# Kernel optimization log

Hardware: AMD Instinct MI355X
Metric: run time of the kernel (lower is better)

## Reference

```python
import jax, jax.numpy as jnp
import numpy as np

B, S, H = 4, 2048, 2048


def _rotate_half(x):
    x1, x2 = jnp.split(x, 2, axis=-1)
    return jnp.concatenate((-x2, x1), axis=-1)


def _rope_tables(seq_len, dim, dtype):
    # standard RoPE over the full hidden dim (emb last dim == dim so it
    # broadcasts against [B,S,dim] activations)
    inv_freq = 1.0 / (10000.0 ** (jnp.arange(0, dim, 2, dtype=jnp.float32) / dim))
    t = jnp.arange(seq_len, dtype=jnp.float32)
    freqs = jnp.einsum('s,d->sd', t, inv_freq)          # [S, dim/2]
    emb = jnp.concatenate((freqs, freqs), axis=-1)      # [S, dim]
    return jnp.cos(emb).astype(dtype)[None], jnp.sin(emb).astype(dtype)[None]  # [1,S,dim]


def setup_inputs() -> dict:
    key = jax.random.key(0)
    ks = jax.random.split(key, 11)
    sc = 0.02
    return {
        'query': jax.random.normal(ks[0], (B, S, H), jnp.float32),
        'key':   jax.random.normal(ks[1], (B, S, H), jnp.float32),
        'value': jax.random.normal(ks[2], (B, S, H), jnp.float32),
        'Wq': jax.random.normal(ks[3], (H, H), jnp.float32) * sc,
        'bq': jax.random.normal(ks[4], (H,), jnp.float32) * sc,
        'Wk': jax.random.normal(ks[5], (H, H), jnp.float32) * sc,
        'bk': jax.random.normal(ks[6], (H,), jnp.float32) * sc,
        'Wv': jax.random.normal(ks[7], (H, H), jnp.float32) * sc,
        'bv': jax.random.normal(ks[8], (H,), jnp.float32) * sc,
        'Wo': jax.random.normal(ks[9], (H, H), jnp.float32) * sc,
        'bo': jax.random.normal(ks[10], (H,), jnp.float32) * sc,
    }


def reference(query, key, value, Wq, bq, Wk, bk, Wv, bv, Wo, bo):
    seq, dim = query.shape[1], query.shape[2]
    cos, sin = _rope_tables(seq, dim, query.dtype)      # [1,S,H]
    q_rot = query * cos + _rotate_half(query) * sin     # RoPE BEFORE projections
    k_rot = key * cos + _rotate_half(key) * sin
    q = jnp.einsum('bsh,oh->bso', q_rot, Wq) + bq       # torch Linear: x @ W.T + b
    k = jnp.einsum('bsh,oh->bso', k_rot, Wk) + bk
    v = jnp.einsum('bsh,oh->bso', value, Wv) + bv
    scale = 1.0 / jnp.sqrt(jnp.asarray(dim, q.dtype))
    scores = jnp.einsum('bqh,bkh->bqk', q, k) * scale   # [B,Sq,Sk]
    probs = jax.nn.softmax(scores, axis=-1)
    context = jnp.einsum('bqk,bkh->bqh', probs, v)
    return jnp.einsum('bsh,oh->bso', context, Wo) + bo
```

## Files before the change

### kernel.cpp

```cpp
#include <hip/hip_runtime.h>


typedef __bf16 bf16_t;
typedef bf16_t bf16x8 __attribute__((ext_vector_type(8)));
typedef bf16_t bf16x4 __attribute__((ext_vector_type(4)));
typedef float  f32x4  __attribute__((ext_vector_type(4)));

#define BDIM 4
#define SDIM 2048
#define HDIM 2048

__device__ __forceinline__ void async_copy16(const bf16_t* g, bf16_t* l) {
  __builtin_amdgcn_global_load_lds(
      (__attribute__((address_space(1))) const void*)g,
      (__attribute__((address_space(3))) void*)l,
      16, 0, 0);
}

__global__ __launch_bounds__(256) void prep_kernel(
    const float* __restrict__ q, const float* __restrict__ k,
    const float* __restrict__ v,
    bf16_t* __restrict__ qr, bf16_t* __restrict__ kr, bf16_t* __restrict__ vb) {
  const int i = blockIdx.x * 256 + threadIdx.x;
  const int j = i & 1023;
  const int row = i >> 10;
  const int s = row & (SDIM - 1);
  const float invf = exp2f(-(float)j * 0.012976281620653759f);
  const float f = (float)s * invf;
  float sn, cs;
  sincosf(f, &sn, &cs);
  const long base = (long)row * HDIM;
  const float q1 = q[base + j], q2 = q[base + j + 1024];
  const float k1 = k[base + j], k2 = k[base + j + 1024];
  qr[base + j]        = (bf16_t)(q1 * cs - q2 * sn);
  qr[base + j + 1024] = (bf16_t)(q2 * cs + q1 * sn);
  kr[base + j]        = (bf16_t)(k1 * cs - k2 * sn);
  kr[base + j + 1024] = (bf16_t)(k2 * cs + k1 * sn);
  vb[base + j]        = (bf16_t)v[base + j];
  vb[base + j + 1024] = (bf16_t)v[base + j + 1024];
}

__global__ __launch_bounds__(256) void wcast_kernel(
    const float* __restrict__ w0, const float* __restrict__ w1,
    const float* __restrict__ w2, const float* __restrict__ w3,
    bf16_t* __restrict__ dst) {
  const int wsel = blockIdx.y;
  const float* src = wsel == 0 ? w0 : wsel == 1 ? w1 : wsel == 2 ? w2 : w3;
  const long i = (long)(blockIdx.x * 256 + threadIdx.x) * 8;
  const float4 a = *(const float4*)&src[i];
  const float4 b = *(const float4*)&src[i + 4];
  bf16x8 o;
  o[0] = (bf16_t)a.x; o[1] = (bf16_t)a.y; o[2] = (bf16_t)a.z; o[3] = (bf16_t)a.w;
  o[4] = (bf16_t)b.x; o[5] = (bf16_t)b.y; o[6] = (bf16_t)b.z; o[7] = (bf16_t)b.w;
  *(bf16x8*)&dst[(long)wsel * HDIM * HDIM + i] = o;
}

__device__ __forceinline__ void stage_A_unit(const bf16_t* __restrict__ G, int K,
                                             int kq, bf16_t* L, int half,
                                             int wave, int rl, int ccs) {
#pragma unroll
  for (int c = 0; c < 2; ++c) {
    const int idx = c * 8 + wave;
    const int g = (idx >> 3) * 16 + (idx & 7) + half * 8;
    async_copy16(G + (long)(g * 8 + rl) * K + kq + ccs, L + g * 512);
  }
}
__device__ __forceinline__ void stage_B_unit(const bf16_t* __restrict__ G, int K,
                                             int kq, bf16_t* L, int half,
                                             int wave, int rl, int ccs) {
#pragma unroll
  for (int c = 0; c < 2; ++c) {
    const int idx = c * 8 + wave;
    const int g = (idx >> 2) * 8 + (idx & 3) + half * 4;
    async_copy16(G + (long)(g * 8 + rl) * K + kq + ccs, L + g * 512);
  }
}

template <int OMODE>
__global__ __launch_bounds__(512, 2) void gemm_bt(
    const bf16_t* __restrict__ A, const bf16_t* __restrict__ Bt,
    void* __restrict__ Cv, const float* __restrict__ bias,
    int M, int N, int K, float alpha,
    long sA, long sB, long sC) {
  __shared__ __align__(16) bf16_t lds[4 * 16384];
  bf16_t* As0 = lds;
  bf16_t* Bs0 = lds + 16384;
  bf16_t* As1 = lds + 32768;
  bf16_t* Bs1 = lds + 49152;
  const int z = blockIdx.z;
  A  += (long)z * sA;
  Bt += (long)z * sB;
  const int tid  = threadIdx.x;
  const int lane = tid & 63;
  const int wave = tid >> 6;
  const int wm = (wave >> 2) * 128;
  const int wn = (wave & 3) * 64;
  const int m0 = blockIdx.y * 256;
  const int n0 = blockIdx.x * 256;
  const int lrow = lane & 15;
  const int quad = lane >> 4;
  const int rl  = lane >> 3;
  const int ccs = ((lane & 7) ^ rl) * 8;

  const bf16_t* Ab = A  + (long)m0 * K;
  const bf16_t* Bb = Bt + (long)n0 * K;

  f32x4 acc[8][4] = {};

#define DS_A(AS, MH)                                                         \
  _Pragma("unroll") for (int ks = 0; ks < 2; ++ks) {                         \
    const int cg = ks * 4 + quad;                                            \
    _Pragma("unroll") for (int t = 0; t < 4; ++t) {                          \
      const int r = wm + ((MH) * 4 + t) * 16 + lrow;                         \
      af[t][ks] = *(const bf16x8*)&(AS)[r * 64 + ((cg ^ (r & 7)) * 8)];      \
    }                                                                        \
  }
#define DS_B(BS, NH)                                                         \
  _Pragma("unroll") for (int ks = 0; ks < 2; ++ks) {                         \
    const int cg = ks * 4 + quad;                                            \
    _Pragma("unroll") for (int u = 0; u < 2; ++u) {                          \
      const int r = wn + ((NH) * 2 + u) * 16 + lrow;                         \
      bfr[u][ks] = *(const bf16x8*)&(BS)[r * 64 + ((cg ^ (r & 7)) * 8)];     \
    }                                                                        \
  }
#define MFMA_Q(MH, NH)                                                       \
  __builtin_amdgcn_s_barrier();                                              \
  asm volatile("s_waitcnt lgkmcnt(0)" ::: "memory");                         \
  __builtin_amdgcn_s_setprio(1);                                             \
  _Pragma("unroll") for (int ks = 0; ks < 2; ++ks)                           \
    _Pragma("unroll") for (int t = 0; t < 4; ++t)                            \
      _Pragma("unroll") for (int u = 0; u < 2; ++u)                          \
        acc[(MH) * 4 + t][(NH) * 2 + u] =                                    \
            __builtin_amdgcn_mfma_f32_16x16x32_bf16(                         \
                af[t][ks], bfr[u][ks], acc[(MH) * 4 + t][(NH) * 2 + u],      \
                0, 0, 0);                                                    \
  __builtin_amdgcn_s_setprio(0);
#define VM_WAIT4 asm volatile("s_waitcnt vmcnt(4)" ::: "memory");
#define ENDBAR   __builtin_amdgcn_s_barrier();

  stage_A_unit(Ab, K, 0,  As0, 0, wave, rl, ccs);
  stage_A_unit(Ab, K, 0,  As0, 1, wave, rl, ccs);
  stage_B_unit(Bb, K, 0,  Bs0, 0, wave, rl, ccs);
  stage_B_unit(Bb, K, 0,  Bs0, 1, wave, rl, ccs);
  stage_A_unit(Ab, K, 64, As1, 0, wave, rl, ccs);
  stage_B_unit(Bb, K, 64, Bs1, 0, wave, rl, ccs);
  asm volatile("s_waitcnt vmcnt(4)" ::: "memory");
  __builtin_amdgcn_s_barrier();

  const int Km = K - 1;
  for (int k0 = 0; k0 < K; k0 += 128) {
    bf16x8 af[4][2], bfr[2][2];
    const int kA = k0 + 64;
    const int kB = (k0 + 128) & Km;
    const int kC = (k0 + 192) & Km;
    DS_A(As0, 0) DS_B(Bs0, 0)
    stage_A_unit(Ab, K, kA, As1, 1, wave, rl, ccs);
    MFMA_Q(0, 0) ENDBAR
    DS_B(Bs0, 1)
    stage_B_unit(Bb, K, kA, Bs1, 1, wave, rl, ccs);
    MFMA_Q(0, 1) ENDBAR
    DS_A(As0, 1) DS_B(Bs0, 0)
    stage_A_unit(Ab, K, kB, As0, 0, wave, rl, ccs);
    MFMA_Q(1, 0) ENDBAR
    DS_B(Bs0, 1)
    stage_B_unit(Bb, K, kB, Bs0, 0, wave, rl, ccs);
    MFMA_Q(1, 1) VM_WAIT4 ENDBAR
    DS_A(As1, 0) DS_B(Bs1, 0)
    stage_A_unit(Ab, K, kB, As0, 1, wave, rl, ccs);
    MFMA_Q(0, 0) ENDBAR
    DS_B(Bs1, 1)
    stage_B_unit(Bb, K, kB, Bs0, 1, wave, rl, ccs);
    MFMA_Q(0, 1) ENDBAR
    DS_A(As1, 1) DS_B(Bs1, 0)
    stage_A_unit(Ab, K, kC, As1, 0, wave, rl, ccs);
    MFMA_Q(1, 0) ENDBAR
    DS_B(Bs1, 1)
    stage_B_unit(Bb, K, kC, Bs1, 0, wave, rl, ccs);
    MFMA_Q(1, 1) VM_WAIT4 ENDBAR
  }
#undef DS_A
#undef DS_B
#undef MFMA_Q
#undef VM_WAIT4
#undef ENDBAR

#pragma unroll
  for (int mt = 0; mt < 8; ++mt) {
#pragma unroll
    for (int nt = 0; nt < 4; ++nt) {
      const int col = n0 + wn + nt * 16 + lrow;
      const float bv = bias ? bias[col] : 0.0f;
      if (OMODE == 2) {
        const int row0 = m0 + wm + mt * 16 + quad * 4;
        const int b = row0 >> 11;
        const int s = row0 & (SDIM - 1);
        bf16x4 o;
#pragma unroll
        for (int r = 0; r < 4; ++r) o[r] = (bf16_t)(acc[mt][nt][r] + bv);
        *(bf16x4*)&((bf16_t*)Cv)[(long)b * SDIM * HDIM + (long)col * SDIM + s] = o;
      } else {
#pragma unroll
        for (int r = 0; r < 4; ++r) {
          const int row = m0 + wm + mt * 16 + quad * 4 + r;
          const float v = acc[mt][nt][r] * alpha + bv;
          if (OMODE == 1)
            ((float*)Cv)[(long)z * sC + (long)row * N + col] = v;
          else
            ((bf16_t*)Cv)[(long)z * sC + (long)row * N + col] = (bf16_t)v;
        }
      }
    }
  }
}

__global__ __launch_bounds__(256) void softmax_kernel(
    const bf16_t* __restrict__ Sc, bf16_t* __restrict__ P) {
  const long row = blockIdx.x;
  const bf16_t* src = Sc + row * SDIM;
  bf16_t* dst = P + row * SDIM;
  const int tid = threadIdx.x;
  const bf16x8 in = *(const bf16x8*)&src[tid * 8];
  float x[8];
#pragma unroll
  for (int t = 0; t < 8; ++t) x[t] = (float)in[t];
  float m = x[0];
#pragma unroll
  for (int t = 1; t < 8; ++t) m = fmaxf(m, x[t]);
#pragma unroll
  for (int off = 32; off; off >>= 1) m = fmaxf(m, __shfl_xor(m, off));
  __shared__ float redm[4], reds[4];
  const int wave = tid >> 6, lane = tid & 63;
  if (lane == 0) redm[wave] = m;
  __syncthreads();
  m = fmaxf(fmaxf(redm[0], redm[1]), fmaxf(redm[2], redm[3]));
  float s = 0.0f;
#pragma unroll
  for (int t = 0; t < 8; ++t) { x[t] = __expf(x[t] - m); s += x[t]; }
#pragma unroll
  for (int off = 32; off; off >>= 1) s += __shfl_xor(s, off);
  if (lane == 0) reds[wave] = s;
  __syncthreads();
  s = reds[0] + reds[1] + reds[2] + reds[3];
  const float inv = 1.0f / s;
  bf16x8 o;
#pragma unroll
  for (int t = 0; t < 8; ++t) o[t] = (bf16_t)(x[t] * inv);
  *(bf16x8*)&dst[tid * 8] = o;
}

extern "C" void kernel_launch(void* const* d_in, const int* in_sizes, int n_in,
                              void* d_out, int out_size, void* d_ws, size_t ws_size,
                              hipStream_t stream) {
  const float* q_in = (const float*)d_in[0];
  const float* k_in = (const float*)d_in[1];
  const float* v_in = (const float*)d_in[2];
  const float* Wq = (const float*)d_in[3];
  const float* bq = (const float*)d_in[4];
  const float* Wk = (const float*)d_in[5];
  const float* bk = (const float*)d_in[6];
  const float* Wv = (const float*)d_in[7];
  const float* bv = (const float*)d_in[8];
  const float* Wo = (const float*)d_in[9];
  const float* bo = (const float*)d_in[10];
  float* out = (float*)d_out;

  const size_t ELE  = (size_t)BDIM * SDIM * HDIM;
  const size_t WELE = (size_t)HDIM * HDIM;
  const size_t SEG  = ELE * 2;

  uint8_t* w = (uint8_t*)d_ws;
  bf16_t* qr  = (bf16_t*)(w + 0 * SEG);
  bf16_t* kr  = (bf16_t*)(w + 1 * SEG);
  bf16_t* vb  = (bf16_t*)(w + 2 * SEG);
  bf16_t* Wb  = (bf16_t*)(w + 3 * SEG);
  bf16_t* qp  = (bf16_t*)(w + 4 * SEG);
  bf16_t* kp  = (bf16_t*)(w + 5 * SEG);
  bf16_t* vpT = (bf16_t*)(w + 6 * SEG);
  bf16_t* scores = (bf16_t*)(w + 0 * SEG);
  bf16_t* probs  = (bf16_t*)(w + 2 * SEG);
  bf16_t* ctx    = (bf16_t*)(w + 1 * SEG);

  bf16_t* Wqb = Wb + 0 * WELE;
  bf16_t* Wkb = Wb + 1 * WELE;
  bf16_t* Wvb = Wb + 2 * WELE;
  bf16_t* Wob = Wb + 3 * WELE;

  const dim3 blk(256);
  const dim3 gblk(512);
  const long SH = (long)SDIM * HDIM;
  const long SS = (long)SDIM * SDIM;

  prep_kernel<<<dim3(ELE / 2 / 256), blk, 0, stream>>>(q_in, k_in, v_in, qr, kr, vb);
  wcast_kernel<<<dim3(WELE / 8 / 256, 4), blk, 0, stream>>>(Wq, Wk, Wv, Wo, Wb);
  gemm_bt<0><<<dim3(8, 32, 1), gblk, 0, stream>>>(qr, Wqb, qp, bq,
      BDIM * SDIM, HDIM, HDIM, 1.0f, 0, 0, 0);
  gemm_bt<0><<<dim3(8, 32, 1), gblk, 0, stream>>>(kr, Wkb, kp, bk,
      BDIM * SDIM, HDIM, HDIM, 1.0f, 0, 0, 0);
  gemm_bt<2><<<dim3(8, 32, 1), gblk, 0, stream>>>(vb, Wvb, vpT, bv,
      BDIM * SDIM, HDIM, HDIM, 1.0f, 0, 0, 0);
  gemm_bt<0><<<dim3(8, 8, BDIM), gblk, 0, stream>>>(qp, kp, scores, nullptr,
      SDIM, SDIM, HDIM, 0.022097086912079612f, SH, SH, SS);
  softmax_kernel<<<dim3(BDIM * SDIM), blk, 0, stream>>>(scores, probs);
  gemm_bt<0><<<dim3(8, 8, BDIM), gblk, 0, stream>>>(probs, vpT, ctx, nullptr,
      SDIM, HDIM, SDIM, 1.0f, SS, SH, SH);
  gemm_bt<1><<<dim3(8, 32, 1), gblk, 0, stream>>>(ctx, Wob, out, bo,
      BDIM * SDIM, HDIM, HDIM, 1.0f, 0, 0, 0);
}
```

Baseline: 653.7 us.

## Stage GEMM epilogue through LDS for coalesced vector global stores

For non-transposed outputs the MFMA operands are swapped so each lane holds four consecutive columns, which enables vector bias loads. Every wave then writes its accumulator tile into a padded per-wave LDS scratch region. It reads the tile back as row-contiguous 16-byte chunks and issues coalesced global stores, replacing the scalar strided stores of the previous epilogue. The shared buffer grows to 144 KiB, so occupancy may drop from two blocks per CU.

```diff
diff --git a/kernel.cpp b/kernel.cpp
--- a/kernel.cpp
+++ b/kernel.cpp
@@ -82,11 +82,11 @@
     void* __restrict__ Cv, const float* __restrict__ bias,
     int M, int N, int K, float alpha,
     long sA, long sB, long sC) {
-  __shared__ __align__(16) bf16_t lds[4 * 16384];
-  bf16_t* As0 = lds;
-  bf16_t* Bs0 = lds + 16384;
-  bf16_t* As1 = lds + 32768;
-  bf16_t* Bs1 = lds + 49152;
+  __shared__ __align__(16) uint8_t smem[147456];
+  bf16_t* As0 = (bf16_t*)smem;
+  bf16_t* Bs0 = (bf16_t*)(smem + 32768);
+  bf16_t* As1 = (bf16_t*)(smem + 65536);
+  bf16_t* Bs1 = (bf16_t*)(smem + 98304);
   const int z = blockIdx.z;
   A  += (long)z * sA;
   Bt += (long)z * sB;
@@ -129,11 +129,14 @@
   __builtin_amdgcn_s_setprio(1);                                             \
   _Pragma("unroll") for (int ks = 0; ks < 2; ++ks)                           \
     _Pragma("unroll") for (int t = 0; t < 4; ++t)                            \
-      _Pragma("unroll") for (int u = 0; u < 2; ++u)                          \
-        acc[(MH) * 4 + t][(NH) * 2 + u] =                                    \
-            __builtin_amdgcn_mfma_f32_16x16x32_bf16(                         \
-                af[t][ks], bfr[u][ks], acc[(MH) * 4 + t][(NH) * 2 + u],      \
-                0, 0, 0);                                                    \
+      _Pragma("unroll") for (int u = 0; u < 2; ++u) {                        \
+        if constexpr (OMODE == 2)                                            \
+          acc[(MH)*4+t][(NH)*2+u] = __builtin_amdgcn_mfma_f32_16x16x32_bf16( \
+              af[t][ks], bfr[u][ks], acc[(MH)*4+t][(NH)*2+u], 0, 0, 0);      \
+        else                                                                 \
+          acc[(MH)*4+t][(NH)*2+u] = __builtin_amdgcn_mfma_f32_16x16x32_bf16( \
+              bfr[u][ks], af[t][ks], acc[(MH)*4+t][(NH)*2+u], 0, 0, 0);      \
+      }                                                                      \
   __builtin_amdgcn_s_setprio(0);
 #define VM_WAIT4 asm volatile("s_waitcnt vmcnt(4)" ::: "memory");
 #define ENDBAR   __builtin_amdgcn_s_barrier();
@@ -184,31 +187,81 @@
 #undef VM_WAIT4
 #undef ENDBAR
 
-#pragma unroll
-  for (int mt = 0; mt < 8; ++mt) {
-#pragma unroll
-    for (int nt = 0; nt < 4; ++nt) {
-      const int col = n0 + wn + nt * 16 + lrow;
-      const float bv = bias ? bias[col] : 0.0f;
-      if (OMODE == 2) {
-        const int row0 = m0 + wm + mt * 16 + quad * 4;
-        const int b = row0 >> 11;
-        const int s = row0 & (SDIM - 1);
+  asm volatile("s_waitcnt vmcnt(0)" ::: "memory");
+  __builtin_amdgcn_s_barrier();
+  uint8_t* smem_w = smem + wave * 18432;
+
+  if constexpr (OMODE == 0) {
+    bf16_t* E = (bf16_t*)smem_w;
+#pragma unroll
+    for (int mt = 0; mt < 8; ++mt)
+#pragma unroll
+      for (int nt = 0; nt < 4; ++nt) {
+        const int nq = nt * 16 + quad * 4;
+        f32x4 bv = {0.0f, 0.0f, 0.0f, 0.0f};
+        if (bias) bv = *(const f32x4*)&bias[n0 + wn + nq];
         bf16x4 o;
 #pragma unroll
+        for (int r = 0; r < 4; ++r)
+          o[r] = (bf16_t)(acc[mt][nt][r] * alpha + bv[r]);
+        *(bf16x4*)&E[(mt * 16 + lrow) * 72 + nq] = o;
+      }
+    const int r8 = lane >> 3, jc = lane & 7;
+    bf16_t* Cb = (bf16_t*)Cv + (long)z * sC + n0 + wn + jc * 8;
+#pragma unroll
+    for (int p = 0; p < 16; ++p) {
+      const int row = p * 8 + r8;
+      const bf16x8 vv = *(const bf16x8*)&E[row * 72 + jc * 8];
+      *(bf16x8*)&Cb[(long)(m0 + wm + row) * N] = vv;
+    }
+  } else if constexpr (OMODE == 1) {
+    float* E = (float*)smem_w;
+    const int r4 = lane >> 4, jc = lane & 15;
+#pragma unroll
+    for (int P = 0; P < 2; ++P) {
+      if (P) asm volatile("s_waitcnt lgkmcnt(0)" ::: "memory");
+#pragma unroll
+      for (int t4 = 0; t4 < 4; ++t4)
+#pragma unroll
+        for (int nt = 0; nt < 4; ++nt) {
+          const int nq = nt * 16 + quad * 4;
+          f32x4 bv = {0.0f, 0.0f, 0.0f, 0.0f};
+          if (bias) bv = *(const f32x4*)&bias[n0 + wn + nq];
+          f32x4 o = acc[P * 4 + t4][nt];
+#pragma unroll
+          for (int r = 0; r < 4; ++r) o[r] = o[r] * alpha + bv[r];
+          *(f32x4*)&E[(t4 * 16 + lrow) * 68 + nq] = o;
+        }
+      float* Cb = (float*)Cv + (long)z * sC + n0 + wn + jc * 4;
+#pragma unroll
+      for (int p = 0; p < 16; ++p) {
+        const int row = p * 4 + r4;
+        const f32x4 vv = *(const f32x4*)&E[row * 68 + jc * 4];
+        *(f32x4*)&Cb[(long)(m0 + wm + P * 64 + row) * N] = vv;
+      }
+    }
+  } else {
+    bf16_t* E = (bf16_t*)smem_w;
+#pragma unroll
+    for (int mt = 0; mt < 8; ++mt)
+#pragma unroll
+      for (int nt = 0; nt < 4; ++nt) {
+        const int h = nt * 16 + lrow;
+        const float bv = bias ? bias[n0 + wn + h] : 0.0f;
+        bf16x4 o;
+#pragma unroll
         for (int r = 0; r < 4; ++r) o[r] = (bf16_t)(acc[mt][nt][r] + bv);
-        *(bf16x4*)&((bf16_t*)Cv)[(long)b * SDIM * HDIM + (long)col * SDIM + s] = o;
-      } else {
-#pragma unroll
-        for (int r = 0; r < 4; ++r) {
-          const int row = m0 + wm + mt * 16 + quad * 4 + r;
-          const float v = acc[mt][nt][r] * alpha + bv;
-          if (OMODE == 1)
-            ((float*)Cv)[(long)z * sC + (long)row * N + col] = v;
-          else
-            ((bf16_t*)Cv)[(long)z * sC + (long)row * N + col] = (bf16_t)v;
-        }
+        *(bf16x4*)&E[h * 136 + mt * 16 + quad * 4] = o;
       }
+    const int r4 = lane >> 4, jc = lane & 15;
+    const int bb = (m0 + wm) >> 11;
+    const int s0 = (m0 + wm) & (SDIM - 1);
+    bf16_t* Ob = (bf16_t*)Cv + (long)bb * SDIM * HDIM + s0 + jc * 8;
+#pragma unroll
+    for (int p = 0; p < 16; ++p) {
+      const int h = p * 4 + r4;
+      const bf16x8 vv = *(const bf16x8*)&E[h * 136 + jc * 8];
+      *(bf16x8*)&Ob[(long)(n0 + wn + h) * SDIM] = vv;
     }
   }
 }
```

Result: no change. 661.9 us (+1.3%).
